# Kernel tuning notes

Hardware: AMD Instinct MI355X
Metric: run time of the kernel (lower is better)

## Reference

```python
import jax, jax.numpy as jnp
import numpy as np

K_SIZE, STRIDE, PAD = 3, 1, 1
B, C1, C2, H, W = 2, 256, 256, 64, 64


def conv2d(x, w, b, stride, pad):
    out = jax.lax.conv_general_dilated(
        x, w, (stride, stride), [(pad, pad), (pad, pad)],
        dimension_numbers=("NCHW", "OIHW", "NCHW"))
    return out + b[None, :, None, None]


def deform_conv2d(x, offset, mask, w, b, k, stride, pad):
    # torchvision.ops.deform_conv2d semantics (modulated, offset_groups=1)
    Bn, C, Hh, Ww = x.shape
    Ho, Wo = offset.shape[2], offset.shape[3]
    K = k * k
    # offset channels are (dy, dx) interleaved per kernel point
    off = offset.reshape(Bn, K, 2, Ho, Wo)
    dy, dx = off[:, :, 0], off[:, :, 1]          # [B,K,Ho,Wo]
    ki = jnp.arange(k)
    kyy, kxx = jnp.meshgrid(ki, ki, indexing="ij")
    kyy, kxx = kyy.reshape(K), kxx.reshape(K)
    base_y = (jnp.arange(Ho) * stride - pad)[None, :, None] + kyy[:, None, None]  # [K,Ho,1]
    base_x = (jnp.arange(Wo) * stride - pad)[None, None, :] + kxx[:, None, None]  # [K,1,Wo]
    ys = base_y[None].astype(x.dtype) + dy       # [B,K,Ho,Wo]
    xs = base_x[None].astype(x.dtype) + dx
    N = K * Ho * Wo
    ysf, xsf = ys.reshape(Bn, N), xs.reshape(Bn, N)
    y0 = jnp.floor(ysf)
    x0 = jnp.floor(xsf)
    ly, lx = ysf - y0, xsf - x0                  # bilinear fractions
    y0i, x0i = y0.astype(jnp.int32), x0.astype(jnp.int32)
    xf = x.reshape(Bn, C, Hh * Ww)

    def gather(yi, xi):
        valid = (yi >= 0) & (yi < Hh) & (xi >= 0) & (xi < Ww)
        idx = jnp.clip(yi, 0, Hh - 1) * Ww + jnp.clip(xi, 0, Ww - 1)
        v = jnp.take_along_axis(xf, idx[:, None, :], axis=2)  # [B,C,N]
        return v * valid[:, None, :].astype(x.dtype)

    v00 = gather(y0i, x0i)
    v01 = gather(y0i, x0i + 1)
    v10 = gather(y0i + 1, x0i)
    v11 = gather(y0i + 1, x0i + 1)
    wy1, wx1 = ly[:, None], lx[:, None]
    val = (v00 * (1 - wy1) * (1 - wx1) + v01 * (1 - wy1) * wx1 +
           v10 * wy1 * (1 - wx1) + v11 * wy1 * wx1)          # [B,C,N]
    val = val.reshape(Bn, C, K, Ho, Wo) * mask[:, None]       # modulate
    out = jnp.einsum("ock,bckhw->bohw", w.reshape(w.shape[0], C, K), val)
    return out + b[None, :, None, None]


def setup_inputs() -> dict:
    key = jax.random.key(0)
    ks = jax.random.split(key, 6)
    k2 = K_SIZE * K_SIZE
    return {
        "x": jax.random.normal(ks[0], (B, C1, H, W), jnp.float32),
        "offset_feat": jax.random.normal(ks[1], (B, C2, H, W), jnp.float32),
        # offset/mask head conv (zero-init in module; small random so offsets are non-trivial)
        "w_offset_mask": jax.random.normal(ks[2], (3 * k2, C2, K_SIZE, K_SIZE), jnp.float32) * 0.01,
        "b_offset_mask": jax.random.normal(ks[3], (3 * k2,), jnp.float32) * 0.01,
        "w_dcn": jax.random.normal(ks[4], (C2, C1, K_SIZE, K_SIZE), jnp.float32) / np.sqrt(C1 * k2),
        "b_dcn": jax.random.normal(ks[5], (C2,), jnp.float32) * 0.01,
    }


def reference(x, offset_feat, w_offset_mask, b_offset_mask, w_dcn, b_dcn):
    om = conv2d(offset_feat, w_offset_mask, b_offset_mask, STRIDE, PAD)  # [B,3*k*k,Ho,Wo]
    o1, o2, m = jnp.split(om, 3, axis=1)
    offset = jnp.concatenate([o1, o2], axis=1)   # [B,2*k*k,Ho,Wo]
    mask = jax.nn.sigmoid(m)                      # [B,k*k,Ho,Wo]
    return deform_conv2d(x, offset, mask, w_dcn, b_dcn, K_SIZE, STRIDE, PAD)
```

## Files before the change

### kernel.cpp

```cpp
#include <hip/hip_runtime.h>
#include <math.h>

#define BATCH 2
#define CIN   256
#define COUT  256
#define COFF  256
#define HWPIX 4096
#define CKTOT 2304
#define VSTR  40
#define PH    66
#define PHW   4356

typedef __attribute__((ext_vector_type(8))) short short8;
typedef __attribute__((ext_vector_type(8))) unsigned short ushort8;
typedef __attribute__((ext_vector_type(4))) float float4v;

__device__ __forceinline__ unsigned short f2bf(float f) {
    unsigned u = __float_as_uint(f);
    unsigned r = (u + 0x7FFFu + ((u >> 16) & 1u)) >> 16;
    return (unsigned short)r;
}
__device__ __forceinline__ float bf2f(unsigned short h) {
    return __uint_as_float(((unsigned)h) << 16);
}

__global__ __launch_bounds__(256) void prep_kernel(
    const float* __restrict__ x, const float* __restrict__ feat,
    const float* __restrict__ wdcn, const float* __restrict__ wom,
    unsigned short* __restrict__ xTh,
    unsigned short* __restrict__ fh,
    unsigned short* __restrict__ whi,
    unsigned short* __restrict__ wohi)
{
    const int bid = blockIdx.x;
    const int tid = threadIdx.x;

    if (bid < 4096) {
        const bool isx = bid < 2048;
        const int lb = isx ? bid : bid - 2048;
        const int b  = lb >> 10;
        const int r  = lb & 1023;
        const int pt = r >> 3;
        const int ct = r & 7;
        __shared__ float t[32][33];
        const int tx = tid & 31, ty = tid >> 5;
        const float* src = isx ? x : feat;
        const float* sb = src + ((size_t)b * 256 + ct * 32) * HWPIX + pt * 32;
#pragma unroll
        for (int i = ty; i < 32; i += 8)
            t[i][tx] = sb[(size_t)i * HWPIX + tx];
        __syncthreads();
        if (isx) {
            unsigned short* ob = xTh + ((size_t)b * HWPIX + pt * 32) * 256 + ct * 32;
#pragma unroll
            for (int i = ty; i < 32; i += 8)
                ob[(size_t)i * 256 + tx] = f2bf(t[tx][i]);
        } else {
#pragma unroll
            for (int i = ty; i < 32; i += 8) {
                int p = pt * 32 + i;
                int row = (p >> 6) + 1, col = (p & 63) + 1;
                fh[((size_t)b * PHW + row * PH + col) * 256 + ct * 32 + tx]
                    = f2bf(t[tx][i]);
            }
        }
    } else if (bid < 6400) {
        int gid = (bid - 4096) * 256 + tid;
        int cc  = gid & 31;
        int co  = (gid >> 5) & 255;
        int kcb = gid >> 13;
        int k   = kcb >> 3;
        int cb  = kcb & 7;
        float w = wdcn[((size_t)co * 256 + cb * 32 + cc) * 9 + k];
        whi[gid] = f2bf(w);
    } else if (bid < 6688) {
        int gid = (bid - 6400) * 256 + tid;
        int cc  = gid & 31;
        int co  = (gid >> 5) & 31;
        int kcb = gid >> 10;
        int k   = kcb >> 3;
        int cb  = kcb & 7;
        float w = 0.0f;
        if (co < 27) w = wom[(size_t)co * CKTOT + (cb * 32 + cc) * 9 + k];
        wohi[gid] = f2bf(w);
    } else {
        int idx = (bid - 6688) * 256 + tid;
        int b = idx / 66560;
        int r = idx - b * 66560;
        int pidx = r >> 8;
        int c = r & 255;
        int row, col;
        if (pidx < 66)       { row = 0;           col = pidx; }
        else if (pidx < 132) { row = 65;          col = pidx - 66; }
        else if (pidx < 196) { row = pidx - 131;  col = 0; }
        else                 { row = pidx - 195;  col = 65; }
        fh[((size_t)b * PHW + row * PH + col) * 256 + c] = 0;
    }
}

__global__ __launch_bounds__(512, 4) void dcn_fused_kernel(
    const unsigned short* __restrict__ xTh,
    const unsigned short* __restrict__ fh,
    const unsigned short* __restrict__ whi,
    const unsigned short* __restrict__ wohi,
    const float* __restrict__ bom,
    const float* __restrict__ bdcn,
    float* __restrict__ out)
{
    const int tid = threadIdx.x;
    const int y   = blockIdx.x >> 1;
    const int xh  = blockIdx.x & 1;
    const int b   = blockIdx.y;

    __shared__ float red[8][32][32];
    __shared__ float4 s_wt[288];
    __shared__ int4   s_ix[288];
    __shared__ unsigned short V[288 * VSTR];

    const int wv   = tid >> 6;
    const int lane = tid & 63;
    const int l15  = lane & 15;
    const int q    = lane >> 4;

    {
        float4v aco[2][2];
#pragma unroll
        for (int t = 0; t < 2; ++t)
#pragma unroll
            for (int p = 0; p < 2; ++p) aco[t][p] = (float4v)0.0f;

        const unsigned short* fhb = fh + (size_t)b * PHW * 256;
#pragma unroll 3
        for (int i = 0; i < 9; ++i) {
            int kcb = wv * 9 + i;
            int k  = kcb >> 3;
            int cb = kcb & 7;
            size_t s = ((size_t)((y + k / 3) * PH + xh * 32 + (k % 3))) * 256
                     + cb * 32 + q * 8;
            short8 bh0 = *(const short8*)(fhb + s + (size_t)l15 * 256);
            short8 bh1 = *(const short8*)(fhb + s + (size_t)(16 + l15) * 256);
            short8 ah0 = *(const short8*)(wohi + ((size_t)kcb * 32 + l15) * 32 + q * 8);
            short8 ah1 = *(const short8*)(wohi + ((size_t)kcb * 32 + 16 + l15) * 32 + q * 8);
            aco[0][0] = __builtin_amdgcn_mfma_f32_16x16x32_bf16(ah0, bh0, aco[0][0], 0, 0, 0);
            aco[0][1] = __builtin_amdgcn_mfma_f32_16x16x32_bf16(ah0, bh1, aco[0][1], 0, 0, 0);
            aco[1][0] = __builtin_amdgcn_mfma_f32_16x16x32_bf16(ah1, bh0, aco[1][0], 0, 0, 0);
            aco[1][1] = __builtin_amdgcn_mfma_f32_16x16x32_bf16(ah1, bh1, aco[1][1], 0, 0, 0);
        }
#pragma unroll
        for (int t = 0; t < 2; ++t)
#pragma unroll
            for (int p = 0; p < 2; ++p)
#pragma unroll
                for (int r = 0; r < 4; ++r)
                    red[wv][t * 16 + q * 4 + r][p * 16 + l15] = aco[t][p][r];
    }
    __syncthreads();

    if (tid < 288) {
        int k   = tid >> 5;
        int pxl = tid & 31;
        float dy = bom[2 * k], dx = bom[2 * k + 1], mm = bom[18 + k];
#pragma unroll
        for (int g = 0; g < 8; ++g) {
            dy += red[g][2 * k][pxl];
            dx += red[g][2 * k + 1][pxl];
            mm += red[g][18 + k][pxl];
        }
        int xx = xh * 32 + pxl;
        float ys = (float)(y  - 1 + (k / 3)) + dy;
        float xs = (float)(xx - 1 + (k % 3)) + dx;
        float y0f = floorf(ys), x0f = floorf(xs);
        int y0 = (int)y0f, x0 = (int)x0f;
        float ly = ys - y0f, lx = xs - x0f;
        float m  = 1.0f / (1.0f + expf(-mm));
        bool yv0 = ((unsigned)y0 < 64u), yv1 = ((unsigned)(y0 + 1) < 64u);
        bool xv0 = ((unsigned)x0 < 64u), xv1 = ((unsigned)(x0 + 1) < 64u);
        int i00 = (y0 * 64 + x0) << 8;
        float4 wt;
        int4 ix;
        wt.x = (yv0 && xv0) ? (1.0f - ly) * (1.0f - lx) * m : 0.0f;
        wt.y = (yv0 && xv1) ? (1.0f - ly) * lx * m          : 0.0f;
        wt.z = (yv1 && xv0) ? ly * (1.0f - lx) * m          : 0.0f;
        wt.w = (yv1 && xv1) ? ly * lx * m                   : 0.0f;
        ix.x = (yv0 && xv0) ? i00          : 0;
        ix.y = (yv0 && xv1) ? i00 + 256    : 0;
        ix.z = (yv1 && xv0) ? i00 + 16384  : 0;
        ix.w = (yv1 && xv1) ? i00 + 16640  : 0;
        s_wt[tid] = wt;
        s_ix[tid] = ix;
    }
    __syncthreads();

    const int w = tid >> 6;

    const int cg   = tid & 3;
    const int spx  = (tid >> 2) & 31;
    const int tapg = tid >> 7;

    float4v acc[2][2];
#pragma unroll
    for (int t = 0; t < 2; ++t)
#pragma unroll
        for (int p = 0; p < 2; ++p) acc[t][p] = (float4v)0.0f;

    const unsigned short* xb = xTh + ((size_t)b << 12) * 256;

    for (int cb = 0; cb < 8; ++cb) {
        {
            const unsigned short* xc = xb + cb * 32 + cg * 8;
#pragma unroll 3
            for (int j = 0; j < 3; ++j) {
                int k = tapg + 4 * j;
                if (k > 8) break;
                int cidx = k * 32 + spx;
                float4 wt = s_wt[cidx];
                int4   ix = s_ix[cidx];
                ushort8 u00 = *(const ushort8*)(xc + ix.x);
                ushort8 u01 = *(const ushort8*)(xc + ix.y);
                ushort8 u10 = *(const ushort8*)(xc + ix.z);
                ushort8 u11 = *(const ushort8*)(xc + ix.w);
                unsigned hv[4];
#pragma unroll
                for (int jj = 0; jj < 4; ++jj) {
                    float va = wt.x * bf2f(u00[2 * jj])     + wt.y * bf2f(u01[2 * jj])
                             + wt.z * bf2f(u10[2 * jj])     + wt.w * bf2f(u11[2 * jj]);
                    float vb = wt.x * bf2f(u00[2 * jj + 1]) + wt.y * bf2f(u01[2 * jj + 1])
                             + wt.z * bf2f(u10[2 * jj + 1]) + wt.w * bf2f(u11[2 * jj + 1]);
                    hv[jj] = (unsigned)f2bf(va) | ((unsigned)f2bf(vb) << 16);
                }
                *(uint4*)&V[cidx * VSTR + cg * 8]
                    = make_uint4(hv[0], hv[1], hv[2], hv[3]);
            }
        }
        __syncthreads();

#pragma unroll 3
        for (int k = 0; k < 9; ++k) {
            const int kcb = k * 8 + cb;
            size_t base = ((size_t)kcb * 256 + w * 32 + l15) * 32 + q * 8;
            short8 ah0 = *(const short8*)(whi + base);
            short8 ah1 = *(const short8*)(whi + base + 16 * 32);
            short8 bh0 = *(const short8*)&V[(k * 32 + l15) * VSTR + q * 8];
            short8 bh1 = *(const short8*)&V[(k * 32 + 16 + l15) * VSTR + q * 8];
            acc[0][0] = __builtin_amdgcn_mfma_f32_16x16x32_bf16(ah0, bh0, acc[0][0], 0, 0, 0);
            acc[0][1] = __builtin_amdgcn_mfma_f32_16x16x32_bf16(ah0, bh1, acc[0][1], 0, 0, 0);
            acc[1][0] = __builtin_amdgcn_mfma_f32_16x16x32_bf16(ah1, bh0, acc[1][0], 0, 0, 0);
            acc[1][1] = __builtin_amdgcn_mfma_f32_16x16x32_bf16(ah1, bh1, acc[1][1], 0, 0, 0);
        }
        __syncthreads();
    }

#pragma unroll
    for (int t = 0; t < 2; ++t) {
#pragma unroll
        for (int r = 0; r < 4; ++r) {
            int co = w * 32 + t * 16 + q * 4 + r;
            float bias = bdcn[co];
#pragma unroll
            for (int p = 0; p < 2; ++p) {
                int px = xh * 32 + p * 16 + l15;
                out[(((size_t)b * COUT + co) << 12) + y * 64 + px]
                    = acc[t][p][r] + bias;
            }
        }
    }
}

extern "C" void kernel_launch(void* const* d_in, const int* in_sizes, int n_in,
                              void* d_out, int out_size, void* d_ws, size_t ws_size,
                              hipStream_t stream)
{
    const float* x    = (const float*)d_in[0];
    const float* feat = (const float*)d_in[1];
    const float* wom  = (const float*)d_in[2];
    const float* bom  = (const float*)d_in[3];
    const float* wdcn = (const float*)d_in[4];
    const float* bdcn = (const float*)d_in[5];
    float* out = (float*)d_out;

    unsigned short* whi  = (unsigned short*)d_ws;
    unsigned short* wohi = whi + (size_t)CKTOT * 256;
    unsigned short* xTh  = wohi + 73728;
    unsigned short* fh   = xTh + (size_t)2 * HWPIX * 256;

    prep_kernel<<<7208, 256, 0, stream>>>(x, feat, wdcn, wom, xTh, fh,
                                          whi, wohi);

    dim3 grid(128, 2);
    dcn_fused_kernel<<<grid, 512, 0, stream>>>(xTh, fh, whi, wohi,
                                               bom, bdcn, out);
}
```

Baseline: 125.0 us.

## Double-buffer deformable gather with register prefetch of next channel block

The bilinear gather loads for channel block cb+1 are now issued into registers while block cb is interpolated and fed to the MFMA loop. The interpolated tile V is double-buffered in shared memory, which removes the trailing barrier per iteration. Shared memory is repacked into one aliased buffer, with the offset-conv reduction scratch overlapping V, and launch bounds are relaxed from 4 to 2 blocks per SM to make room for the extra prefetch registers. The cost is higher register use and lower allowed occupancy.

New measurement: 119.9 us. 4.0% less time.

```diff
diff --git a/kernel.cpp b/kernel.cpp
--- a/kernel.cpp
+++ b/kernel.cpp
@@ -4,12 +4,12 @@
 #define BATCH 2
 #define CIN   256
 #define COUT  256
-#define COFF  256
 #define HWPIX 4096
 #define CKTOT 2304
 #define VSTR  40
 #define PH    66
 #define PHW   4356
+#define VBUF  (288 * VSTR)
 
 typedef __attribute__((ext_vector_type(8))) short short8;
 typedef __attribute__((ext_vector_type(8))) unsigned short ushort8;
@@ -98,7 +98,7 @@
     }
 }
 
-__global__ __launch_bounds__(512, 4) void dcn_fused_kernel(
+__global__ __launch_bounds__(512, 2) void dcn_fused_kernel(
     const unsigned short* __restrict__ xTh,
     const unsigned short* __restrict__ fh,
     const unsigned short* __restrict__ whi,
@@ -112,10 +112,11 @@
     const int xh  = blockIdx.x & 1;
     const int b   = blockIdx.y;
 
-    __shared__ float red[8][32][32];
-    __shared__ float4 s_wt[288];
-    __shared__ int4   s_ix[288];
-    __shared__ unsigned short V[288 * VSTR];
+    __shared__ __align__(16) char smem[2 * VBUF * 2 + 288 * 16 + 288 * 16];
+    float (*red)[32][32]   = (float (*)[32][32])smem;
+    unsigned short* V      = (unsigned short*)smem;
+    float4* s_wt           = (float4*)(smem + 2 * VBUF * 2);
+    int4*   s_ix           = (int4*)(smem + 2 * VBUF * 2 + 288 * 16);
 
     const int wv   = tid >> 6;
     const int lane = tid & 63;
@@ -203,35 +204,51 @@
 #pragma unroll
         for (int p = 0; p < 2; ++p) acc[t][p] = (float4v)0.0f;
 
-    const unsigned short* xb = xTh + ((size_t)b << 12) * 256;
+    const unsigned short* xc0 = xTh + ((size_t)b << 12) * 256 + cg * 8;
+
+    ushort8 pf[3][4];
+
+    auto gload = [&](int cb) {
+        const unsigned short* xc = xc0 + cb * 32;
+#pragma unroll
+        for (int j = 0; j < 3; ++j) {
+            int k = tapg + 4 * j;
+            if (k > 8) continue;
+            int cidx = k * 32 + spx;
+            int4 ix = s_ix[cidx];
+            pf[j][0] = *(const ushort8*)(xc + ix.x);
+            pf[j][1] = *(const ushort8*)(xc + ix.y);
+            pf[j][2] = *(const ushort8*)(xc + ix.z);
+            pf[j][3] = *(const ushort8*)(xc + ix.w);
+        }
+    };
+    auto interp = [&](int buf) {
+#pragma unroll
+        for (int j = 0; j < 3; ++j) {
+            int k = tapg + 4 * j;
+            if (k > 8) continue;
+            int cidx = k * 32 + spx;
+            float4 wt = s_wt[cidx];
+            unsigned hv[4];
+#pragma unroll
+            for (int jj = 0; jj < 4; ++jj) {
+                float va = wt.x * bf2f(pf[j][0][2 * jj])     + wt.y * bf2f(pf[j][1][2 * jj])
+                         + wt.z * bf2f(pf[j][2][2 * jj])     + wt.w * bf2f(pf[j][3][2 * jj]);
+                float vb = wt.x * bf2f(pf[j][0][2 * jj + 1]) + wt.y * bf2f(pf[j][1][2 * jj + 1])
+                         + wt.z * bf2f(pf[j][2][2 * jj + 1]) + wt.w * bf2f(pf[j][3][2 * jj + 1]);
+                hv[jj] = (unsigned)f2bf(va) | ((unsigned)f2bf(vb) << 16);
+            }
+            *(uint4*)&V[buf * VBUF + cidx * VSTR + cg * 8]
+                = make_uint4(hv[0], hv[1], hv[2], hv[3]);
+        }
+    };
+
+    gload(0);
 
     for (int cb = 0; cb < 8; ++cb) {
-        {
-            const unsigned short* xc = xb + cb * 32 + cg * 8;
-#pragma unroll 3
-            for (int j = 0; j < 3; ++j) {
-                int k = tapg + 4 * j;
-                if (k > 8) break;
-                int cidx = k * 32 + spx;
-                float4 wt = s_wt[cidx];
-                int4   ix = s_ix[cidx];
-                ushort8 u00 = *(const ushort8*)(xc + ix.x);
-                ushort8 u01 = *(const ushort8*)(xc + ix.y);
-                ushort8 u10 = *(const ushort8*)(xc + ix.z);
-                ushort8 u11 = *(const ushort8*)(xc + ix.w);
-                unsigned hv[4];
-#pragma unroll
-                for (int jj = 0; jj < 4; ++jj) {
-                    float va = wt.x * bf2f(u00[2 * jj])     + wt.y * bf2f(u01[2 * jj])
-                             + wt.z * bf2f(u10[2 * jj])     + wt.w * bf2f(u11[2 * jj]);
-                    float vb = wt.x * bf2f(u00[2 * jj + 1]) + wt.y * bf2f(u01[2 * jj + 1])
-                             + wt.z * bf2f(u10[2 * jj + 1]) + wt.w * bf2f(u11[2 * jj + 1]);
-                    hv[jj] = (unsigned)f2bf(va) | ((unsigned)f2bf(vb) << 16);
-                }
-                *(uint4*)&V[cidx * VSTR + cg * 8]
-                    = make_uint4(hv[0], hv[1], hv[2], hv[3]);
-            }
-        }
+        const int buf = cb & 1;
+        interp(buf);
+        if (cb < 7) gload(cb + 1);
         __syncthreads();
 
 #pragma unroll 3
@@ -240,14 +257,13 @@
             size_t base = ((size_t)kcb * 256 + w * 32 + l15) * 32 + q * 8;
             short8 ah0 = *(const short8*)(whi + base);
             short8 ah1 = *(const short8*)(whi + base + 16 * 32);
-            short8 bh0 = *(const short8*)&V[(k * 32 + l15) * VSTR + q * 8];
-            short8 bh1 = *(const short8*)&V[(k * 32 + 16 + l15) * VSTR + q * 8];
+            short8 bh0 = *(const short8*)&V[buf * VBUF + (k * 32 + l15) * VSTR + q * 8];
+            short8 bh1 = *(const short8*)&V[buf * VBUF + (k * 32 + 16 + l15) * VSTR + q * 8];
             acc[0][0] = __builtin_amdgcn_mfma_f32_16x16x32_bf16(ah0, bh0, acc[0][0], 0, 0, 0);
             acc[0][1] = __builtin_amdgcn_mfma_f32_16x16x32_bf16(ah0, bh1, acc[0][1], 0, 0, 0);
             acc[1][0] = __builtin_amdgcn_mfma_f32_16x16x32_bf16(ah1, bh0, acc[1][0], 0, 0, 0);
             acc[1][1] = __builtin_amdgcn_mfma_f32_16x16x32_bf16(ah1, bh1, acc[1][1], 0, 0, 0);
         }
-        __syncthreads();
     }
 
 #pragma unroll
```
